# Kernel tuning notes

Measured on AMD Instinct MI355X. Metric: run time of the kernel, lower is better.

The kernel has to match this reference:

```python
import jax, jax.numpy as jnp
import numpy as np

N_NODES = 100000
N_EDGES = 1280000
D_IN = 64
D_HID = 64


def _sage_conv(x, src, dst, deg, Wl, bl, Wr):
    # gather source-node features per edge, scatter-mean to destination nodes
    msg = x[src]                                            # [E, d]
    agg = jax.ops.segment_sum(msg, dst, num_segments=N_NODES)  # [N, d]
    mean = agg / deg                                        # [N, d]
    # PyG SAGEConv: lin_l(aggregated) + lin_r(root); bias lives in lin_l
    return mean @ Wl.T + bl + x @ Wr.T


def setup_inputs() -> dict:
    key = jax.random.key(0)
    ks = jax.random.split(key, 10)
    x = jax.random.normal(ks[0], (N_NODES, D_IN), dtype=jnp.float32)
    edge_index = jax.random.randint(ks[1], (2, N_EDGES), 0, N_NODES, dtype=jnp.int64)
    s = 1.0 / np.sqrt(D_IN)
    W1l = jax.random.uniform(ks[2], (D_HID, D_IN), jnp.float32, -s, s)
    W1r = jax.random.uniform(ks[3], (D_HID, D_IN), jnp.float32, -s, s)
    b1 = jax.random.uniform(ks[4], (D_HID,), jnp.float32, -s, s)
    s2 = 1.0 / np.sqrt(D_HID)
    W2l = jax.random.uniform(ks[5], (D_HID, D_HID), jnp.float32, -s2, s2)
    W2r = jax.random.uniform(ks[6], (D_HID, D_HID), jnp.float32, -s2, s2)
    b2 = jax.random.uniform(ks[7], (D_HID,), jnp.float32, -s2, s2)
    Wh = jax.random.uniform(ks[8], (1, D_HID), jnp.float32, -s2, s2)
    bh = jax.random.uniform(ks[9], (1,), jnp.float32, -s2, s2)
    return {"x": x, "edge_index": edge_index, "W1l": W1l, "W1r": W1r, "b1": b1,
            "W2l": W2l, "W2r": W2r, "b2": b2, "Wh": Wh, "bh": bh}


def reference(x, edge_index, W1l, W1r, b1, W2l, W2r, b2, Wh, bh):
    src, dst = edge_index[0], edge_index[1]
    # in-degree for mean aggregation (clamped to avoid div-by-zero)
    deg = jax.ops.segment_sum(jnp.ones((N_EDGES,), jnp.float32), dst,
                              num_segments=N_NODES)
    deg = jnp.maximum(deg, 1.0)[:, None]                    # [N, 1]
    h = jax.nn.relu(_sage_conv(x, src, dst, deg, W1l, b1, W1r))
    h = jax.nn.relu(_sage_conv(h, src, dst, deg, W2l, b2, W2r))
    out = (h @ Wh.T + bh)[:, 0]                             # [N]
    return out, h
```

## Files before the change

kernel.cpp:

```cpp
#include <hip/hip_runtime.h>

#define N_NODES 100000
#define N_EDGES 1280000
#define D 64
#define NPAD 102400
#define CAP 48
#define NBUCK 391
#define AB 313
#define NT16 6250
#define XQ (N_NODES * 16)
#define CVTOT (XQ + 32 + 4096)
#define SPLIT 720000
#define CV1 384
#define CV2 384

typedef __attribute__((ext_vector_type(8))) short bf16x8;
typedef __attribute__((ext_vector_type(4))) float f32x4;
typedef __attribute__((ext_vector_type(2))) float f32x2;

__device__ __forceinline__ unsigned short f2bf(float f) {
    union { float f; unsigned u; } c; c.f = f;
    unsigned u = c.u;
    return (unsigned short)((u + 0x7FFF + ((u >> 16) & 1)) >> 16);
}
__device__ __forceinline__ float fp8d(unsigned b) {
    unsigned t = ((b & 0x80u) << 24) | ((b & 0x7fu) << 20);
    union { unsigned u; float f; } c; c.u = t;
    return c.f * 1.32922799578491587e36f;
}
__device__ __forceinline__ unsigned char f2fp8(float f) {
    f = fminf(fmaxf(f, -448.f), 448.f);
    float g = f * 7.52316384526264005e-37f;
    union { float f; unsigned u; } c; c.f = g;
    unsigned gb = c.u;
    unsigned r = (((gb & 0x7fffffffu) + 0x7ffffu + ((gb >> 20) & 1u)) >> 20) & 0x7fu;
    return (unsigned char)(((gb >> 24) & 0x80u) | r);
}

__device__ __forceinline__ void cvt_range(
    int gtid, int gsz, int lo0, int hi,
    const float* __restrict__ x,
    const float* __restrict__ W1l, const float* __restrict__ W1r,
    const float* __restrict__ W2l, const float* __restrict__ W2r,
    unsigned short* __restrict__ xb, unsigned short* __restrict__ h1b,
    unsigned char* __restrict__ x8, unsigned char* __restrict__ h8,
    unsigned short* __restrict__ wb)
{
    for (int i = lo0 + gtid; i < hi; i += gsz) {
        if (i < XQ) {
            float4 v = ((const float4*)x)[i];
            ((ushort4*)xb)[i] = make_ushort4(f2bf(v.x), f2bf(v.y), f2bf(v.z), f2bf(v.w));
            ((uchar4*)x8)[i]  = make_uchar4(f2fp8(v.x), f2fp8(v.y), f2fp8(v.z), f2fp8(v.w));
        } else if (i < XQ + 32) {
            int k = i - XQ;
            if (k < 16) {
                ((ushort4*)xb)[(size_t)N_NODES * 16 + k] = make_ushort4(0,0,0,0);
                ((unsigned*)x8)[(size_t)N_NODES * 16 + k] = 0u;
            } else {
                ((ushort4*)h1b)[(size_t)N_NODES * 16 + (k - 16)] = make_ushort4(0,0,0,0);
                ((unsigned*)h8)[(size_t)N_NODES * 16 + (k - 16)] = 0u;
            }
        } else {
            int wf = i - XQ - 32;
            int m = wf >> 10, k = wf & 1023;
            const float* s = (m == 0) ? W1l : (m == 1) ? W1r : (m == 2) ? W2l : W2r;
            float4 v = ((const float4*)s)[k];
            ((ushort4*)wb)[m * 1024 + k] =
                make_ushort4(f2bf(v.x), f2bf(v.y), f2bf(v.z), f2bf(v.w));
        }
    }
}

__global__ __launch_bounds__(512) void prep_kernel(
    const float* __restrict__ x,
    const int* __restrict__ src, const int* __restrict__ dst,
    const float* __restrict__ W1l, const float* __restrict__ W1r,
    const float* __restrict__ W2l, const float* __restrict__ W2r,
    unsigned short* __restrict__ xb, unsigned short* __restrict__ h1b,
    unsigned char* __restrict__ x8, unsigned char* __restrict__ h8,
    unsigned short* __restrict__ wb,
    int* __restrict__ sorted, int* __restrict__ exclT)
{
    __shared__ int cntA[392];
    __shared__ int excl[392];
    __shared__ int stage_pk[4096];

    const int t   = threadIdx.x;
    const int bid = blockIdx.x;

    if (bid < AB) {
        const int e0 = bid * 4096;
        const int cbatch = min(4096, N_EDGES - e0);

        if (t < 392) cntA[t] = 0;
        __syncthreads();

        int mb[8], mr[8], mpk[8];
#pragma unroll
        for (int i = 0; i < 8; ++i) {
            int idx = i * 512 + t;
            mb[i] = -1;
            if (idx < cbatch) {
                int e = e0 + idx;
                int s = src[e], d = dst[e];
                int b = d >> 8;
                mb[i]  = b;
                mpk[i] = (s << 8) | (d & 255);
                mr[i]  = atomicAdd(&cntA[b], 1);
            }
        }
        __syncthreads();

        if (t < 64) {
            int pre[7], tot = 0;
            if (t < 56) {
#pragma unroll
                for (int i = 0; i < 7; ++i) { pre[i] = tot; tot += cntA[t * 7 + i]; }
            }
            int sc = tot;
#pragma unroll
            for (int off = 1; off < 64; off <<= 1) {
                int u = __shfl_up(sc, off, 64);
                if (t >= off) sc += u;
            }
            int ex = sc - tot;
            if (t < 56) {
#pragma unroll
                for (int i = 0; i < 7; ++i) excl[t * 7 + i] = ex + pre[i];
            }
        }
        __syncthreads();

#pragma unroll
        for (int i = 0; i < 8; ++i) {
            if (mb[i] >= 0)
                stage_pk[excl[mb[i]] + mr[i]] = mpk[i];
        }
        __syncthreads();

#pragma unroll
        for (int i = 0; i < 8; ++i) {
            int idx = i * 512 + t;
            if (idx < cbatch) sorted[e0 + idx] = stage_pk[idx];
        }
        if (t < 392) exclT[bid * 392 + t] = excl[t];
    } else {
        const int gtid = (bid - AB) * 512 + t;
        cvt_range(gtid, CV1 * 512, 0, SPLIT,
                  x, W1l, W1r, W2l, W2r, xb, h1b, x8, h8, wb);
    }
}

__global__ __launch_bounds__(512) void binB_kernel(
    const int* __restrict__ sorted, const int* __restrict__ exclT,
    int* __restrict__ csr, int* __restrict__ deg,
    const float* __restrict__ x,
    const float* __restrict__ W1l, const float* __restrict__ W1r,
    const float* __restrict__ W2l, const float* __restrict__ W2r,
    unsigned short* __restrict__ xb, unsigned short* __restrict__ h1b,
    unsigned char* __restrict__ x8, unsigned char* __restrict__ h8,
    unsigned short* __restrict__ wb)
{
    __shared__ int cur[256];
    __shared__ __align__(16) int lcsr[256 * CAP];

    const int t = threadIdx.x;
    const int k = blockIdx.x;

    if (k < NBUCK) {
        if (t < 256) cur[t] = 0;
        __syncthreads();

        for (int u = t; u < 2 * AB; u += 512) {
            int seg = u >> 1, half = u & 1;
            int s0  = exclT[seg * 392 + k];
            int cnt = exclT[seg * 392 + k + 1] - s0;
            int b0 = half ? (cnt >> 1) : 0;
            int b1 = half ? cnt : (cnt >> 1);
            const int* sp = sorted + seg * 4096 + s0 + b0;
            int m = b1 - b0;
            if (m > 0) {
                int pk = sp[0];
                for (int e = 0; e < m; ++e) {
                    int nxt = (e + 1 < m) ? sp[e + 1] : 0;
                    int nl = pk & 255;
                    int r  = atomicAdd(&cur[nl], 1);
                    if (r < CAP) lcsr[nl * CAP + r] = pk >> 8;
                    pk = nxt;
                }
            }
        }
        __syncthreads();

        const int base = k * 256;
        for (int i = t; i < 4096; i += 512) {
            int r = i >> 4, cc = i & 15;
            if (cc < 12) {
                int lenr = min(cur[r], CAP);
                if (cc * 4 < lenr)
                    *(int4*)(csr + (size_t)(base + r) * CAP + cc * 4) =
                        *(const int4*)(lcsr + r * CAP + cc * 4);
            }
        }
        if (t < 256) deg[base + t] = cur[t];
    } else {
        const int gtid = (k - NBUCK) * 512 + t;
        cvt_range(gtid, CV2 * 512, SPLIT, CVTOT,
                  x, W1l, W1r, W2l, W2r, xb, h1b, x8, h8, wb);
    }
}

template <int LAYER>
__global__ __launch_bounds__(256) void layer_kernel(
    const int* __restrict__ csr, const int* __restrict__ deg_g,
    const unsigned char*  __restrict__ feat8,
    const unsigned short* __restrict__ root_b,
    const unsigned short* __restrict__ wl_b,
    const float* __restrict__ bl,
    const unsigned short* __restrict__ wr_b,
    unsigned short* __restrict__ hout_b,
    unsigned char*  __restrict__ hout8,
    float* __restrict__ hout_f,
    const float* __restrict__ Wh, const float* __restrict__ bh,
    float* __restrict__ out)
{
    __shared__ __align__(16) char lds[5120];
    unsigned short* sA = (unsigned short*)lds;
    unsigned short* sX = sA + 16 * 72;
    float* sH    = (float*)lds;
    float* spart = (float*)(lds + 4608);

    const int tid = threadIdx.x;
    const int n0  = blockIdx.x * 16;

    const int jt = tid >> 6;
    const int l64 = tid & 63;
    const int rowl = l64 & 15, quad = l64 >> 4;
    const unsigned short* wlp = wl_b + (jt * 16 + rowl) * 64 + quad * 8;
    const unsigned short* wrp = wr_b + (jt * 16 + rowl) * 64 + quad * 8;
    bf16x8 b0 = *(const bf16x8*)(wlp);
    bf16x8 b1 = *(const bf16x8*)(wlp + 32);
    bf16x8 b2 = *(const bf16x8*)(wrp);
    bf16x8 b3 = *(const bf16x8*)(wrp + 32);
    float bj = bl[jt * 16 + rowl];

    {
        int row = tid >> 4, c4 = tid & 15;
        ushort4 x4 = ((const ushort4*)root_b)[(n0 + row) * 16 + c4];
        *(ushort4*)(sX + row * 72 + c4 * 4) = x4;
    }

    {
        const uint2* fb2 = (const uint2*)feat8;
        const int g   = tid >> 4;
        const int l   = tid & 15;
        const int h   = l >> 3;
        const int lo  = l & 7;
        const int n   = n0 + g;
        const int* rp = csr + (size_t)n * CAP;
        const int dg  = deg_g[n];
        const int id0 = rp[l];
        const int len = (dg < CAP) ? dg : CAP;
        f32x2 a0 = {0.f, 0.f}, a1 = {0.f, 0.f}, a2 = {0.f, 0.f}, a3 = {0.f, 0.f};

#if __has_builtin(__builtin_amdgcn_cvt_pk_f32_fp8)
#define GCHUNK(IDEXPR)                                                       \
        {                                                                    \
            int id_ = (IDEXPR);                                              \
            uint2 w[8];                                                      \
            _Pragma("unroll")                                                \
            for (int i = 0; i < 8; ++i)                                      \
                w[i] = fb2[(__shfl(id_, 2 * i + h, 16) << 3) + lo];          \
            _Pragma("unroll")                                                \
            for (int i = 0; i < 8; ++i) {                                    \
                a0 += __builtin_amdgcn_cvt_pk_f32_fp8((int)w[i].x, false);   \
                a1 += __builtin_amdgcn_cvt_pk_f32_fp8((int)w[i].x, true);    \
                a2 += __builtin_amdgcn_cvt_pk_f32_fp8((int)w[i].y, false);   \
                a3 += __builtin_amdgcn_cvt_pk_f32_fp8((int)w[i].y, true);    \
            }                                                                \
        }
#else
#define GCHUNK(IDEXPR)                                                       \
        {                                                                    \
            int id_ = (IDEXPR);                                              \
            uint2 w[8];                                                      \
            _Pragma("unroll")                                                \
            for (int i = 0; i < 8; ++i)                                      \
                w[i] = fb2[(__shfl(id_, 2 * i + h, 16) << 3) + lo];          \
            _Pragma("unroll")                                                \
            for (int i = 0; i < 8; ++i) {                                    \
                f32x2 p0 = {fp8d(w[i].x & 255), fp8d((w[i].x >> 8) & 255)};  \
                f32x2 p1 = {fp8d((w[i].x >> 16) & 255), fp8d(w[i].x >> 24)}; \
                f32x2 p2 = {fp8d(w[i].y & 255), fp8d((w[i].y >> 8) & 255)};  \
                f32x2 p3 = {fp8d((w[i].y >> 16) & 255), fp8d(w[i].y >> 24)}; \
                a0 += p0; a1 += p1; a2 += p2; a3 += p3;                      \
            }                                                                \
        }
#endif

        GCHUNK((l < len) ? id0 : N_NODES);
        for (int cb = 16; cb < len; cb += 16) {
            int idxl = cb + l;
            GCHUNK((idxl < len) ? rp[idxl] : N_NODES);
        }
#undef GCHUNK

        a0.x += __shfl_xor(a0.x, 8); a0.y += __shfl_xor(a0.y, 8);
        a1.x += __shfl_xor(a1.x, 8); a1.y += __shfl_xor(a1.y, 8);
        a2.x += __shfl_xor(a2.x, 8); a2.y += __shfl_xor(a2.y, 8);
        a3.x += __shfl_xor(a3.x, 8); a3.y += __shfl_xor(a3.y, 8);
        float inv = 1.0f / fmaxf((float)dg, 1.0f);
        if (h == 0) {
            *(ushort4*)(sA + g * 72 + lo * 8) =
                make_ushort4(f2bf(a0.x * inv), f2bf(a0.y * inv),
                             f2bf(a1.x * inv), f2bf(a1.y * inv));
            *(ushort4*)(sA + g * 72 + lo * 8 + 4) =
                make_ushort4(f2bf(a2.x * inv), f2bf(a2.y * inv),
                             f2bf(a3.x * inv), f2bf(a3.y * inv));
        }
    }
    __syncthreads();

    const unsigned short* ap = sA + rowl * 72 + quad * 8;
    const unsigned short* xp = sX + rowl * 72 + quad * 8;
    bf16x8 am0 = *(const bf16x8*)(ap);
    bf16x8 am1 = *(const bf16x8*)(ap + 32);
    bf16x8 ax0 = *(const bf16x8*)(xp);
    bf16x8 ax1 = *(const bf16x8*)(xp + 32);
    __syncthreads();

    f32x4 acc = {0.f, 0.f, 0.f, 0.f};
    acc = __builtin_amdgcn_mfma_f32_16x16x32_bf16(am0, b0, acc, 0, 0, 0);
    acc = __builtin_amdgcn_mfma_f32_16x16x32_bf16(am1, b1, acc, 0, 0, 0);
    acc = __builtin_amdgcn_mfma_f32_16x16x32_bf16(ax0, b2, acc, 0, 0, 0);
    acc = __builtin_amdgcn_mfma_f32_16x16x32_bf16(ax1, b3, acc, 0, 0, 0);

#pragma unroll
    for (int r = 0; r < 4; ++r) {
        int node = quad * 4 + r;
        sH[node * 68 + jt * 16 + rowl] = fmaxf(acc[r] + bj, 0.f);
    }
    __syncthreads();

    if (LAYER == 2 && tid < 128) {
        int node = tid >> 3, q = tid & 7;
        float p = 0.f;
#pragma unroll
        for (int c = 0; c < 2; ++c) {
            float4 hv = *(const float4*)(sH + node * 68 + q * 8 + c * 4);
            float4 wv = ((const float4*)Wh)[q * 2 + c];
            p += hv.x * wv.x + hv.y * wv.y + hv.z * wv.z + hv.w * wv.w;
        }
        spart[tid] = p;
    }

    {
        int row = tid >> 4, c4 = tid & 15;
        int n = n0 + row;
        const float* hp = sH + row * 68 + c4 * 4;
        if (LAYER == 1) {
            ((ushort4*)hout_b)[n * 16 + c4] =
                make_ushort4(f2bf(hp[0]), f2bf(hp[1]), f2bf(hp[2]), f2bf(hp[3]));
            ((uchar4*)hout8)[n * 16 + c4] =
                make_uchar4(f2fp8(hp[0]), f2fp8(hp[1]), f2fp8(hp[2]), f2fp8(hp[3]));
        } else {
            ((float4*)hout_f)[n * 16 + c4] =
                make_float4(hp[0], hp[1], hp[2], hp[3]);
        }
    }

    if (LAYER == 2) {
        __syncthreads();
        if (tid < 16) {
            float s = bh[0];
#pragma unroll
            for (int q = 0; q < 8; ++q) s += spart[tid * 8 + q];
            out[n0 + tid] = s;
        }
    }
}

extern "C" void kernel_launch(void* const* d_in, const int* in_sizes, int n_in,
                              void* d_out, int out_size, void* d_ws, size_t ws_size,
                              hipStream_t stream) {
    const float* x   = (const float*)d_in[0];
    const int*   ei  = (const int*)d_in[1];
    const int*   src = ei;
    const int*   dst = ei + N_EDGES;
    const float* W1l = (const float*)d_in[2];
    const float* W1r = (const float*)d_in[3];
    const float* b1  = (const float*)d_in[4];
    const float* W2l = (const float*)d_in[5];
    const float* W2r = (const float*)d_in[6];
    const float* b2  = (const float*)d_in[7];
    const float* Wh  = (const float*)d_in[8];
    const float* bh  = (const float*)d_in[9];

    float* out   = (float*)d_out;
    float* h_out = out + N_NODES;

    int* wsi = (int*)d_ws;
    int* deg = wsi;
    int* csr = deg + NPAD;
    unsigned short* wb  = (unsigned short*)(csr + NBUCK * 256 * CAP);
    unsigned short* x_b = wb + 16384;
    unsigned short* h1b = x_b + (size_t)(N_NODES + 1) * D;
    unsigned char*  x8  = (unsigned char*)(h1b + (size_t)(N_NODES + 1) * D);
    unsigned char*  h8  = x8 + (size_t)(N_NODES + 1) * D;
    int* sorted = (int*)h1b;
    int* exclT  = sorted + AB * 4096;

    unsigned short* w1l_b = wb;
    unsigned short* w1r_b = wb + 4096;
    unsigned short* w2l_b = wb + 8192;
    unsigned short* w2r_b = wb + 12288;

    prep_kernel<<<AB + CV1, 512, 0, stream>>>(
        x, src, dst, W1l, W1r, W2l, W2r, x_b, h1b, x8, h8, wb, sorted, exclT);

    binB_kernel<<<NBUCK + CV2, 512, 0, stream>>>(
        sorted, exclT, csr, deg,
        x, W1l, W1r, W2l, W2r, x_b, h1b, x8, h8, wb);

    layer_kernel<1><<<NT16, 256, 0, stream>>>(
        csr, deg, x8, x_b, w1l_b, b1, w1r_b, h1b, h8, nullptr,
        nullptr, nullptr, nullptr);
    layer_kernel<2><<<NT16, 256, 0, stream>>>(
        csr, deg, h8, h1b, w2l_b, b2, w2r_b, nullptr, nullptr, h_out,
        Wh, bh, out);
}
```

Measured before the change: 165.3 us.

## Fuse both SAGE layers into one persistent kernel with a grid barrier

Replaces the two separate layer kernel launches with a single persistent kernel that loops over node tiles for layer 1, does a software grid-wide barrier through an atomic counter, then processes layer 2. The grid size comes from an occupancy query so every block is resident, which the barrier needs. This removes one launch and the drain/fill gap between the layers. In exchange it adds a memset for the barrier counter, atomic spinning, and possibly lower occupancy from the launch_bounds hint, and it risks deadlock if not all blocks are co-resident.

```diff
diff --git a/kernel.cpp b/kernel.cpp
--- a/kernel.cpp
+++ b/kernel.cpp
@@ -13,6 +13,7 @@
 #define SPLIT 720000
 #define CV1 384
 #define CV2 384
+#define LGRID 2048
 
 typedef __attribute__((ext_vector_type(8))) short bf16x8;
 typedef __attribute__((ext_vector_type(4))) float f32x4;
@@ -35,6 +36,19 @@
     unsigned gb = c.u;
     unsigned r = (((gb & 0x7fffffffu) + 0x7ffffu + ((gb >> 20) & 1u)) >> 20) & 0x7fu;
     return (unsigned char)(((gb >> 24) & 0x80u) | r);
+}
+
+__device__ __forceinline__ void grid_sync(int* bar, int target) {
+    __syncthreads();
+    if (threadIdx.x == 0) {
+        __threadfence();
+        atomicAdd(bar, 1);
+        while (__hip_atomic_load(bar, __ATOMIC_RELAXED,
+                                 __HIP_MEMORY_SCOPE_AGENT) < target)
+            __builtin_amdgcn_s_sleep(2);
+        __threadfence();
+    }
+    __syncthreads();
 }
 
 __device__ __forceinline__ void cvt_range(
@@ -211,27 +225,20 @@
 }
 
 template <int LAYER>
-__global__ __launch_bounds__(256) void layer_kernel(
-    const int* __restrict__ csr, const int* __restrict__ deg_g,
-    const unsigned char*  __restrict__ feat8,
-    const unsigned short* __restrict__ root_b,
-    const unsigned short* __restrict__ wl_b,
-    const float* __restrict__ bl,
-    const unsigned short* __restrict__ wr_b,
-    unsigned short* __restrict__ hout_b,
-    unsigned char*  __restrict__ hout8,
-    float* __restrict__ hout_f,
-    const float* __restrict__ Wh, const float* __restrict__ bh,
-    float* __restrict__ out)
+__device__ __forceinline__ void layer_tile(int tdx, char* lds,
+    const int* csr, const int* deg_g,
+    const unsigned char* feat8, const unsigned short* root_b,
+    const unsigned short* wl_b, const float* bl, const unsigned short* wr_b,
+    unsigned short* hout_b, unsigned char* hout8, float* hout_f,
+    const float* Wh, const float* bh, float* out)
 {
-    __shared__ __align__(16) char lds[5120];
     unsigned short* sA = (unsigned short*)lds;
     unsigned short* sX = sA + 16 * 72;
     float* sH    = (float*)lds;
     float* spart = (float*)(lds + 4608);
 
     const int tid = threadIdx.x;
-    const int n0  = blockIdx.x * 16;
+    const int n0  = tdx * 16;
 
     const int jt = tid >> 6;
     const int l64 = tid & 63;
@@ -378,6 +385,31 @@
             out[n0 + tid] = s;
         }
     }
+    __syncthreads();
+}
+
+__global__ __launch_bounds__(256, 8) void layers_kernel(
+    const int* __restrict__ csr, const int* __restrict__ deg,
+    const unsigned char* __restrict__ x8, const unsigned short* __restrict__ x_b,
+    unsigned short* __restrict__ h1b, unsigned char* __restrict__ h8,
+    const unsigned short* __restrict__ wb,
+    const float* __restrict__ b1, const float* __restrict__ b2,
+    float* __restrict__ h_out,
+    const float* __restrict__ Wh, const float* __restrict__ bh,
+    float* __restrict__ out, int* bar)
+{
+    __shared__ __align__(16) char lds[5120];
+    const int nb = gridDim.x;
+
+    for (int t = blockIdx.x; t < NT16; t += nb)
+        layer_tile<1>(t, lds, csr, deg, x8, x_b, wb, b1, wb + 4096,
+                      h1b, h8, nullptr, nullptr, nullptr, nullptr);
+
+    grid_sync(bar, nb);
+
+    for (int t = blockIdx.x; t < NT16; t += nb)
+        layer_tile<2>(t, lds, csr, deg, h8, h1b, wb + 8192, b2, wb + 12288,
+                      nullptr, nullptr, h_out, Wh, bh, out);
 }
 
 extern "C" void kernel_launch(void* const* d_in, const int* in_sizes, int n_in,
@@ -400,7 +432,8 @@
     float* h_out = out + N_NODES;
 
     int* wsi = (int*)d_ws;
-    int* deg = wsi;
+    int* bar = wsi;
+    int* deg = wsi + 64;
     int* csr = deg + NPAD;
     unsigned short* wb  = (unsigned short*)(csr + NBUCK * 256 * CAP);
     unsigned short* x_b = wb + 16384;
@@ -410,10 +443,17 @@
     int* sorted = (int*)h1b;
     int* exclT  = sorted + AB * 4096;
 
-    unsigned short* w1l_b = wb;
-    unsigned short* w1r_b = wb + 4096;
-    unsigned short* w2l_b = wb + 8192;
-    unsigned short* w2r_b = wb + 12288;
+    static int nblk = 0;
+    if (nblk == 0) {
+        int nb2 = 0;
+        if (hipOccupancyMaxActiveBlocksPerMultiprocessor(&nb2, layers_kernel, 256, 0)
+                != hipSuccess || nb2 < 1)
+            nb2 = 1;
+        nblk = nb2 * 256;
+        if (nblk > LGRID) nblk = LGRID;
+    }
+
+    hipMemsetAsync(bar, 0, 256, stream);
 
     prep_kernel<<<AB + CV1, 512, 0, stream>>>(
         x, src, dst, W1l, W1r, W2l, W2r, x_b, h1b, x8, h8, wb, sorted, exclT);
@@ -422,10 +462,6 @@
         sorted, exclT, csr, deg,
         x, W1l, W1r, W2l, W2r, x_b, h1b, x8, h8, wb);
 
-    layer_kernel<1><<<NT16, 256, 0, stream>>>(
-        csr, deg, x8, x_b, w1l_b, b1, w1r_b, h1b, h8, nullptr,
-        nullptr, nullptr, nullptr);
-    layer_kernel<2><<<NT16, 256, 0, stream>>>(
-        csr, deg, h8, h1b, w2l_b, b2, w2r_b, nullptr, nullptr, h_out,
-        Wh, bh, out);
-}
+    layers_kernel<<<nblk, 256, 0, stream>>>(
+        csr, deg, x8, x_b, h1b, h8, wb, b1, b2, h_out, Wh, bh, out, bar);
+}
```

New measurement: 334.9 us. 103% more time.
